# Performance work log

Hardware: AMD Instinct MI355X
Metric: run time of the kernel (lower is better)

## Reference

```python
import jax, jax.numpy as jnp
import numpy as np

B, N, D, P = 16, 128, 1024, 128  # batch, seq_len, n_in, n_mlp
SCALE = 0  # scores divided by P**SCALE (supar convention); scale=0 => no-op


def setup_inputs() -> dict:
    key = jax.random.key(0)
    ks = jax.random.split(key, 6)
    s_in = 1.0 / np.sqrt(D)   # keep MLP activations ~unit scale
    s_w = 1.0 / P             # keep triple-product scores bounded
    return {
        "x": jax.random.normal(ks[0], (B, N, D), jnp.float32),
        "x_span": jax.random.normal(ks[1], (B, N, D), jnp.float32),
        # MLP projections (Linear weight stored torch-style as (out, in))
        "Wx": jax.random.normal(ks[2], (P, D), jnp.float32) * s_in,
        "bx": jnp.zeros((P,), jnp.float32),
        "Wy": jax.random.normal(ks[3], (P, D), jnp.float32) * s_in,
        "by": jnp.zeros((P,), jnp.float32),
        "Wz": jax.random.normal(ks[4], (P, D), jnp.float32) * s_in,
        "bz": jnp.zeros((P,), jnp.float32),
        # Triaffine weight: (P+1 [bias_x], P [z, no bias], P+1 [bias_y]), n_out=1 squeezed
        "W3": jax.random.normal(ks[5], (P + 1, P, P + 1), jnp.float32) * s_w,
    }


def _mlp(h, W, b):
    # supar MLP: Linear + LeakyReLU(0.1); dropout=0 at inference
    return jax.nn.leaky_relu(h @ W.T + b, 0.1)


def reference(x, x_span, Wx, bx, Wy, by, Wz, bz, W3):
    xp = _mlp(x_span, Wx, bx)  # (B,N,P)  -> triaffine arg x
    yp = _mlp(x_span, Wy, by)  # (B,N,P)  -> triaffine arg y
    zp = _mlp(x, Wz, bz)       # (B,N,P)  -> triaffine arg z (head words)
    ones = jnp.ones((B, N, 1), xp.dtype)
    x1 = jnp.concatenate([xp, ones], axis=-1)  # bias_x
    y1 = jnp.concatenate([yp, ones], axis=-1)  # bias_y
    # w: per-head-word bilinear map, (B,N,P+1,P+1)
    w = jnp.einsum('bzk,ikj->bzij', zp, W3)
    # s: (B, z, x, y) = (B,N,N,N)
    s = jnp.einsum('bxi,bzij,byj->bzxy', x1, w, y1)
    s = s / (P ** SCALE)
    # Span2oScorer: s.permute(0, 2, 3, 1).float() -> (B, span_i, span_j, head)
    return jnp.transpose(s, (0, 2, 3, 1)).astype(jnp.float32)
```

## Files before the change

kernel.cpp:

```cpp
#include <hip/hip_runtime.h>

typedef __bf16 bf16;
typedef __bf16 bf16x8 __attribute__((ext_vector_type(8)));
typedef __bf16 bf16x4 __attribute__((ext_vector_type(4)));
typedef float f32x4 __attribute__((ext_vector_type(4)));

#define MFMA(a, b, c) __builtin_amdgcn_mfma_f32_16x16x32_bf16((a), (b), (c), 0, 0, 0)

static __device__ __forceinline__ f32x4 zero4() {
    f32x4 z; z[0] = 0.f; z[1] = 0.f; z[2] = 0.f; z[3] = 0.f; return z;
}

static __device__ __forceinline__ void soft_barrier() {
    __builtin_amdgcn_sched_barrier(0);
    asm volatile("s_waitcnt lgkmcnt(0)" ::: "memory");
    __builtin_amdgcn_s_barrier();
    __builtin_amdgcn_sched_barrier(0);
}

__global__ __launch_bounds__(256) void k_prep(
    const float* __restrict__ Wx, const float* __restrict__ Wy, const float* __restrict__ Wz,
    const float* __restrict__ W3,
    bf16* __restrict__ wbf, bf16* __restrict__ w3b, float* __restrict__ w3bias)
{
    const int b = blockIdx.x, t = threadIdx.x;
    if (b < 96) {
        int proj = b >> 5;
        const float* src = (proj == 0) ? Wx : (proj == 1) ? Wy : Wz;
        bf16* dst = wbf + proj * 131072;
        int o = (b & 31) * 4096 + t * 16;
#pragma unroll
        for (int u = 0; u < 4; u++) {
            float4 v = *(const float4*)(src + o + u * 4);
            bf16x4 w; w[0] = (bf16)v.x; w[1] = (bf16)v.y; w[2] = (bf16)v.z; w[3] = (bf16)v.w;
            *(bf16x4*)(dst + o + u * 4) = w;
        }
    } else {
        int nb = b - 96;
        int n = nb * 8 + (t >> 5);
        int c = t & 31;
        const float* row = W3 + n * 129;
        float v0 = row[4 * c + 0];
        float v1 = row[4 * c + 1];
        float v2 = row[4 * c + 2];
        float v3 = row[4 * c + 3];
        bf16x4 w;
        w[0] = (bf16)v0; w[1] = (bf16)v1; w[2] = (bf16)v2; w[3] = (bf16)v3;
        *(bf16x4*)(w3b + n * 136 + 4 * c) = w;
        if (c == 0) w3bias[n] = row[128];
    }
}

__global__ __launch_bounds__(256) void k_mlp(
    const float* __restrict__ xsp, const float* __restrict__ x,
    const bf16* __restrict__ wbf,
    const float* __restrict__ bx, const float* __restrict__ by, const float* __restrict__ bz,
    bf16* __restrict__ pout)
{
    __shared__ bf16 Al[16 * 1032];
    const int proj = blockIdx.y;
    const float* A = (proj == 2) ? x : xsp;
    const bf16* W = wbf + proj * 131072;
    const float* bias = (proj == 0) ? bx : (proj == 1) ? by : bz;
    bf16* out = pout + proj * 262144;

    const int tid = threadIdx.x;
    const int wv = tid >> 6, lane = tid & 63, quad = lane >> 4, lr = lane & 15;
    const int m0 = blockIdx.x * 16;

    {
        const float* Asrc = A + m0 * 1024;
        const int rr = tid >> 7, cc = (tid & 127) * 8;
#pragma unroll
        for (int i = 0; i < 8; i++) {
            int r = i * 2 + rr;
            float4 v0 = *(const float4*)(Asrc + r * 1024 + cc);
            float4 v1 = *(const float4*)(Asrc + r * 1024 + cc + 4);
            bf16x8 w;
            w[0] = (bf16)v0.x; w[1] = (bf16)v0.y; w[2] = (bf16)v0.z; w[3] = (bf16)v0.w;
            w[4] = (bf16)v1.x; w[5] = (bf16)v1.y; w[6] = (bf16)v1.z; w[7] = (bf16)v1.w;
            *(bf16x8*)(&Al[r * 1032 + cc]) = w;
        }
    }
    __syncthreads();

    f32x4 acc[2];
    acc[0] = zero4(); acc[1] = zero4();

    const bf16* brow = Al + lr * 1032 + quad * 8;
    const bf16* arow = W + (wv * 16 + lr) * 1024 + quad * 8;

#pragma unroll 4
    for (int kw = 0; kw < 32; kw++) {
        bf16x8 bfr = *(const bf16x8*)(brow + kw * 32);
        bf16x8 a0 = *(const bf16x8*)(arow + kw * 32);
        bf16x8 a1 = *(const bf16x8*)(arow + 65536 + kw * 32);
        acc[0] = MFMA(a0, bfr, acc[0]);
        acc[1] = MFMA(a1, bfr, acc[1]);
    }
#pragma unroll
    for (int s = 0; s < 2; s++) {
        int p = (wv + s * 4) * 16 + quad * 4;
        float4 bv = *(const float4*)(bias + p);
        int m = m0 + lr;
        bf16x4 o;
        float v0 = acc[s][0] + bv.x; o[0] = (bf16)(v0 > 0.f ? v0 : 0.1f * v0);
        float v1 = acc[s][1] + bv.y; o[1] = (bf16)(v1 > 0.f ? v1 : 0.1f * v1);
        float v2 = acc[s][2] + bv.z; o[2] = (bf16)(v2 > 0.f ? v2 : 0.1f * v2);
        float v3 = acc[s][3] + bv.w; o[3] = (bf16)(v3 > 0.f ? v3 : 0.1f * v3);
        *(bf16x4*)(out + m * 128 + p) = o;
    }
}

__global__ __launch_bounds__(256, 4) void k_vgemm(
    const bf16* __restrict__ yp,
    const bf16* __restrict__ w3b,
    const float* __restrict__ w3bias,
    bf16* __restrict__ V)
{
    __shared__ bf16 Vt[128 * 136];
    const int b = blockIdx.y;
    const int n0 = blockIdx.x * 128;
    const int tid = threadIdx.x;
    const int wv = tid >> 6, lane = tid & 63, quad = lane >> 4, lr = lane & 15;
    const int y0 = wv * 32;

    const bf16* Ab = yp + b * 16384;

    f32x4 acc[8][2];
#pragma unroll
    for (int nt = 0; nt < 8; nt++) { acc[nt][0] = zero4(); acc[nt][1] = zero4(); }

#pragma unroll
    for (int kw = 0; kw < 4; kw++) {
        bf16x8 b0 = *(const bf16x8*)(Ab + (y0 + lr) * 128 + kw * 32 + quad * 8);
        bf16x8 b1 = *(const bf16x8*)(Ab + (y0 + 16 + lr) * 128 + kw * 32 + quad * 8);
#pragma unroll
        for (int nt = 0; nt < 8; nt++) {
            bf16x8 af = *(const bf16x8*)(w3b + (n0 + nt * 16 + lr) * 136 + kw * 32 + quad * 8);
            acc[nt][0] = MFMA(af, b0, acc[nt][0]);
            acc[nt][1] = MFMA(af, b1, acc[nt][1]);
        }
    }
#pragma unroll
    for (int nt = 0; nt < 8; nt++) {
        int nl = nt * 16 + quad * 4;
        float4 bv = *(const float4*)(w3bias + n0 + nl);
#pragma unroll
        for (int s = 0; s < 2; s++) {
            int y = y0 + s * 16 + lr;
            bf16x4 o;
            o[0] = (bf16)(acc[nt][s][0] + bv.x);
            o[1] = (bf16)(acc[nt][s][1] + bv.y);
            o[2] = (bf16)(acc[nt][s][2] + bv.z);
            o[3] = (bf16)(acc[nt][s][3] + bv.w);
            *(bf16x4*)(&Vt[y * 136 + nl]) = o;
        }
    }
    __syncthreads();
    const int yr = tid >> 4, nn = (tid & 15) * 8;
#pragma unroll
    for (int pass = 0; pass < 8; pass++) {
        int y = pass * 16 + yr;
        bf16x8 v = *(const bf16x8*)(&Vt[y * 136 + nn]);
        *(bf16x8*)(V + (b * 128 + y) * 16512 + n0 + nn) = v;
    }
}

__global__ __launch_bounds__(512, 4) void k_score(
    const bf16* __restrict__ xp,
    const bf16* __restrict__ zp,
    const bf16* __restrict__ V,
    float* __restrict__ out)
{
    __shared__ __align__(16) bf16 Vl[2][129 * 136];
    __shared__ float Hb[128];
    const int tid = threadIdx.x;
    const int wv = tid >> 6, lane = tid & 63, quad = lane >> 4, lr = lane & 15;
    const int r0 = wv * 16 + lr;

    const int it0 = blockIdx.x * 4;
    const int b = it0 >> 7;
    const int y0 = it0 & 127;

    const bf16* Zb = zp + b * 16384;
    const bf16* Xb = xp + b * 16384;
    const bf16* Vbase = V + (b * 128 + y0) * 16512;

    bf16x8 st[4], st4;
#pragma unroll
    for (int q = 0; q < 8; q++) st4[q] = (bf16)0.f;
#pragma unroll
    for (int u = 0; u < 4; u++) st[u] = *(const bf16x8*)(Vbase + (tid + u * 512) * 8);
    if (tid < 16) st4 = *(const bf16x8*)(Vbase + (2048 + tid) * 8);

    bf16x8 bz[4], bxf[4];
#pragma unroll
    for (int kw = 0; kw < 4; kw++) bz[kw] = *(const bf16x8*)(Zb + r0 * 128 + kw * 32 + quad * 8);
#pragma unroll
    for (int iw = 0; iw < 4; iw++) bxf[iw] = *(const bf16x8*)(Xb + r0 * 128 + iw * 32 + quad * 8);

#pragma unroll 1
    for (int n = 0; n < 4; n++) {
        bf16* Bc = &Vl[n & 1][0];

#pragma unroll
        for (int u = 0; u < 4; u++) {
            int c = tid + u * 512;
            *(bf16x8*)(Bc + (c >> 4) * 136 + (c & 15) * 8) = st[u];
        }
        if (tid < 16) *(bf16x8*)(Bc + 128 * 136 + tid * 8) = st4;
        soft_barrier();

        f32x4 acc1[9];
#pragma unroll
        for (int it = 0; it < 9; it++) acc1[it] = zero4();

#pragma unroll
        for (int kw = 0; kw < 4; kw++) {
#pragma unroll
            for (int it = 0; it < 8; it++) {
                bf16x8 af = *(const bf16x8*)(Bc + (it * 16 + lr) * 136 + kw * 32 + quad * 8);
                acc1[it] = MFMA(af, bz[kw], acc1[it]);
            }
            bf16x8 a8;
#pragma unroll
            for (int q = 0; q < 8; q++) a8[q] = (bf16)0.f;
            if (lr == 0) a8 = *(const bf16x8*)(Bc + 128 * 136 + kw * 32 + quad * 8);
            acc1[8] = MFMA(a8, bz[kw], acc1[8]);
        }
        soft_barrier();

#pragma unroll
        for (int it = 0; it < 8; it++) {
            int i = it * 16 + quad * 4;
            bf16x4 o;
            o[0] = (bf16)acc1[it][0];
            o[1] = (bf16)acc1[it][1];
            o[2] = (bf16)acc1[it][2];
            o[3] = (bf16)acc1[it][3];
            *(bf16x4*)(Bc + r0 * 136 + i) = o;
        }
        if (quad == 0) Hb[r0] = acc1[8][0];
        soft_barrier();

        if (n < 3) {
            const bf16* Vnx = Vbase + (n + 1) * 16512;
#pragma unroll
            for (int u = 0; u < 4; u++) st[u] = *(const bf16x8*)(Vnx + (tid + u * 512) * 8);
            if (tid < 16) st4 = *(const bf16x8*)(Vnx + (2048 + tid) * 8);
        }

        f32x4 acc2[8];
#pragma unroll
        for (int zt = 0; zt < 8; zt++) acc2[zt] = zero4();

#pragma unroll
        for (int iw = 0; iw < 4; iw++) {
#pragma unroll
            for (int zt = 0; zt < 8; zt++) {
                bf16x8 ah = *(const bf16x8*)(Bc + (zt * 16 + lr) * 136 + iw * 32 + quad * 8);
                acc2[zt] = MFMA(ah, bxf[iw], acc2[zt]);
            }
        }
#pragma unroll
        for (int zt = 0; zt < 8; zt++) {
            int zb = zt * 16 + quad * 4;
            f32x4 hb = *(const f32x4*)(&Hb[zb]);
            f32x4 o;
            o[0] = acc2[zt][0] + hb[0];
            o[1] = acc2[zt][1] + hb[1];
            o[2] = acc2[zt][2] + hb[2];
            o[3] = acc2[zt][3] + hb[3];
            *(f32x4*)(out + (((b * 128 + r0) * 128 + (y0 + n)) * 128 + zb)) = o;
        }
    }
}

extern "C" void kernel_launch(void* const* d_in, const int* in_sizes, int n_in,
                              void* d_out, int out_size, void* d_ws, size_t ws_size,
                              hipStream_t stream) {
    const float* x   = (const float*)d_in[0];
    const float* xsp = (const float*)d_in[1];
    const float* Wx  = (const float*)d_in[2];
    const float* bx  = (const float*)d_in[3];
    const float* Wy  = (const float*)d_in[4];
    const float* by  = (const float*)d_in[5];
    const float* Wz  = (const float*)d_in[6];
    const float* bz  = (const float*)d_in[7];
    const float* W3  = (const float*)d_in[8];
    float* out = (float*)d_out;

    char* ws = (char*)d_ws;
    bf16*  wbf    = (bf16*)(ws + 8388608);
    bf16*  w3b    = (bf16*)(ws + 9175040);
    bf16*  pout   = (bf16*)(ws + 13666304);
    bf16*  V      = (bf16*)(ws + 15239168);
    float* w3bias = (float*)(ws + 82872320);

    k_prep<<<2160, 256, 0, stream>>>(Wx, Wy, Wz, W3, wbf, w3b, w3bias);
    k_mlp<<<dim3(128, 3), 256, 0, stream>>>(xsp, x, wbf, bx, by, bz, pout);
    k_vgemm<<<dim3(129, 16), 256, 0, stream>>>(pout + 262144 , w3b, w3bias, V);
    k_score<<<512, 512, 0, stream>>>(pout , pout + 524288 , V, out);
}
```

Before: 245.8 us.

## Halve k_score block size with two row tiles per wave; reorder vgemm grid

k_score now runs 256 threads per block, and each wave handles 32 rows as two 16-row tiles. Every A-fragment read from LDS therefore feeds two MFMAs, which halves LDS reads per MFMA and doubles the staging registers per thread. Separately, k_vgemm's grid is transposed so consecutive blocks cover different batches of the same W3 column tile, which should improve L2 reuse of w3b. The cost is higher register pressure and fewer waves per block to hide latency.

```diff
diff --git a/kernel.cpp b/kernel.cpp
--- a/kernel.cpp
+++ b/kernel.cpp
@@ -119,8 +119,8 @@
     bf16* __restrict__ V)
 {
     __shared__ bf16 Vt[128 * 136];
-    const int b = blockIdx.y;
-    const int n0 = blockIdx.x * 128;
+    const int b = blockIdx.x;
+    const int n0 = blockIdx.y * 128;
     const int tid = threadIdx.x;
     const int wv = tid >> 6, lane = tid & 63, quad = lane >> 4, lr = lane & 15;
     const int y0 = wv * 32;
@@ -167,7 +167,7 @@
     }
 }
 
-__global__ __launch_bounds__(512, 4) void k_score(
+__global__ __launch_bounds__(256, 2) void k_score(
     const bf16* __restrict__ xp,
     const bf16* __restrict__ zp,
     const bf16* __restrict__ V,
@@ -177,7 +177,7 @@
     __shared__ float Hb[128];
     const int tid = threadIdx.x;
     const int wv = tid >> 6, lane = tid & 63, quad = lane >> 4, lr = lane & 15;
-    const int r0 = wv * 16 + lr;
+    const int c0 = wv * 32;
 
     const int it0 = blockIdx.x * 4;
     const int b = it0 >> 7;
@@ -187,92 +187,111 @@
     const bf16* Xb = xp + b * 16384;
     const bf16* Vbase = V + (b * 128 + y0) * 16512;
 
-    bf16x8 st[4], st4;
+    bf16x8 st[8], st4;
 #pragma unroll
     for (int q = 0; q < 8; q++) st4[q] = (bf16)0.f;
 #pragma unroll
-    for (int u = 0; u < 4; u++) st[u] = *(const bf16x8*)(Vbase + (tid + u * 512) * 8);
+    for (int u = 0; u < 8; u++) st[u] = *(const bf16x8*)(Vbase + (tid + u * 256) * 8);
     if (tid < 16) st4 = *(const bf16x8*)(Vbase + (2048 + tid) * 8);
 
-    bf16x8 bz[4], bxf[4];
-#pragma unroll
-    for (int kw = 0; kw < 4; kw++) bz[kw] = *(const bf16x8*)(Zb + r0 * 128 + kw * 32 + quad * 8);
-#pragma unroll
-    for (int iw = 0; iw < 4; iw++) bxf[iw] = *(const bf16x8*)(Xb + r0 * 128 + iw * 32 + quad * 8);
+    bf16x8 bz[4][2], bxf[4][2];
+#pragma unroll
+    for (int kw = 0; kw < 4; kw++)
+#pragma unroll
+        for (int s = 0; s < 2; s++)
+            bz[kw][s] = *(const bf16x8*)(Zb + (c0 + s * 16 + lr) * 128 + kw * 32 + quad * 8);
+#pragma unroll
+    for (int iw = 0; iw < 4; iw++)
+#pragma unroll
+        for (int s = 0; s < 2; s++)
+            bxf[iw][s] = *(const bf16x8*)(Xb + (c0 + s * 16 + lr) * 128 + iw * 32 + quad * 8);
 
 #pragma unroll 1
     for (int n = 0; n < 4; n++) {
         bf16* Bc = &Vl[n & 1][0];
 
 #pragma unroll
-        for (int u = 0; u < 4; u++) {
-            int c = tid + u * 512;
+        for (int u = 0; u < 8; u++) {
+            int c = tid + u * 256;
             *(bf16x8*)(Bc + (c >> 4) * 136 + (c & 15) * 8) = st[u];
         }
         if (tid < 16) *(bf16x8*)(Bc + 128 * 136 + tid * 8) = st4;
         soft_barrier();
 
-        f32x4 acc1[9];
-#pragma unroll
-        for (int it = 0; it < 9; it++) acc1[it] = zero4();
+        f32x4 acc1[9][2];
+#pragma unroll
+        for (int it = 0; it < 9; it++) { acc1[it][0] = zero4(); acc1[it][1] = zero4(); }
 
 #pragma unroll
         for (int kw = 0; kw < 4; kw++) {
 #pragma unroll
             for (int it = 0; it < 8; it++) {
                 bf16x8 af = *(const bf16x8*)(Bc + (it * 16 + lr) * 136 + kw * 32 + quad * 8);
-                acc1[it] = MFMA(af, bz[kw], acc1[it]);
+                acc1[it][0] = MFMA(af, bz[kw][0], acc1[it][0]);
+                acc1[it][1] = MFMA(af, bz[kw][1], acc1[it][1]);
             }
             bf16x8 a8;
 #pragma unroll
             for (int q = 0; q < 8; q++) a8[q] = (bf16)0.f;
             if (lr == 0) a8 = *(const bf16x8*)(Bc + 128 * 136 + kw * 32 + quad * 8);
-            acc1[8] = MFMA(a8, bz[kw], acc1[8]);
+            acc1[8][0] = MFMA(a8, bz[kw][0], acc1[8][0]);
+            acc1[8][1] = MFMA(a8, bz[kw][1], acc1[8][1]);
         }
         soft_barrier();
 
 #pragma unroll
         for (int it = 0; it < 8; it++) {
             int i = it * 16 + quad * 4;
-            bf16x4 o;
-            o[0] = (bf16)acc1[it][0];
-            o[1] = (bf16)acc1[it][1];
-            o[2] = (bf16)acc1[it][2];
-            o[3] = (bf16)acc1[it][3];
-            *(bf16x4*)(Bc + r0 * 136 + i) = o;
-        }
-        if (quad == 0) Hb[r0] = acc1[8][0];
+#pragma unroll
+            for (int s = 0; s < 2; s++) {
+                bf16x4 o;
+                o[0] = (bf16)acc1[it][s][0];
+                o[1] = (bf16)acc1[it][s][1];
+                o[2] = (bf16)acc1[it][s][2];
+                o[3] = (bf16)acc1[it][s][3];
+                *(bf16x4*)(Bc + (c0 + s * 16 + lr) * 136 + i) = o;
+            }
+        }
+        if (quad == 0) {
+            Hb[c0 + lr]      = acc1[8][0][0];
+            Hb[c0 + 16 + lr] = acc1[8][1][0];
+        }
         soft_barrier();
 
         if (n < 3) {
             const bf16* Vnx = Vbase + (n + 1) * 16512;
 #pragma unroll
-            for (int u = 0; u < 4; u++) st[u] = *(const bf16x8*)(Vnx + (tid + u * 512) * 8);
+            for (int u = 0; u < 8; u++) st[u] = *(const bf16x8*)(Vnx + (tid + u * 256) * 8);
             if (tid < 16) st4 = *(const bf16x8*)(Vnx + (2048 + tid) * 8);
         }
 
-        f32x4 acc2[8];
-#pragma unroll
-        for (int zt = 0; zt < 8; zt++) acc2[zt] = zero4();
+        f32x4 acc2[8][2];
+#pragma unroll
+        for (int zt = 0; zt < 8; zt++) { acc2[zt][0] = zero4(); acc2[zt][1] = zero4(); }
 
 #pragma unroll
         for (int iw = 0; iw < 4; iw++) {
 #pragma unroll
             for (int zt = 0; zt < 8; zt++) {
                 bf16x8 ah = *(const bf16x8*)(Bc + (zt * 16 + lr) * 136 + iw * 32 + quad * 8);
-                acc2[zt] = MFMA(ah, bxf[iw], acc2[zt]);
+                acc2[zt][0] = MFMA(ah, bxf[iw][0], acc2[zt][0]);
+                acc2[zt][1] = MFMA(ah, bxf[iw][1], acc2[zt][1]);
             }
         }
 #pragma unroll
         for (int zt = 0; zt < 8; zt++) {
             int zb = zt * 16 + quad * 4;
             f32x4 hb = *(const f32x4*)(&Hb[zb]);
-            f32x4 o;
-            o[0] = acc2[zt][0] + hb[0];
-            o[1] = acc2[zt][1] + hb[1];
-            o[2] = acc2[zt][2] + hb[2];
-            o[3] = acc2[zt][3] + hb[3];
-            *(f32x4*)(out + (((b * 128 + r0) * 128 + (y0 + n)) * 128 + zb)) = o;
+#pragma unroll
+            for (int s = 0; s < 2; s++) {
+                int xx = c0 + s * 16 + lr;
+                f32x4 o;
+                o[0] = acc2[zt][s][0] + hb[0];
+                o[1] = acc2[zt][s][1] + hb[1];
+                o[2] = acc2[zt][s][2] + hb[2];
+                o[3] = acc2[zt][s][3] + hb[3];
+                *(f32x4*)(out + (((b * 128 + xx) * 128 + (y0 + n)) * 128 + zb)) = o;
+            }
         }
     }
 }
@@ -300,6 +319,6 @@
 
     k_prep<<<2160, 256, 0, stream>>>(Wx, Wy, Wz, W3, wbf, w3b, w3bias);
     k_mlp<<<dim3(128, 3), 256, 0, stream>>>(xsp, x, wbf, bx, by, bz, pout);
-    k_vgemm<<<dim3(129, 16), 256, 0, stream>>>(pout + 262144 , w3b, w3bias, V);
-    k_score<<<512, 512, 0, stream>>>(pout , pout + 524288 , V, out);
-}
+    k_vgemm<<<dim3(16, 129), 256, 0, stream>>>(pout + 262144 , w3b, w3bias, V);
+    k_score<<<512, 256, 0, stream>>>(pout , pout + 524288 , V, out);
+}
```

Measured after the change: 241.3 us, median of 2. Within noise of the previous version (-1.8%).
